# Performance work log

Measured on AMD Instinct MI355X. Metric: run time of the kernel, lower is better.

## Reference

```python
import jax, jax.numpy as jnp
import numpy as np
import math

B, T, D = 2, 4096, 2048
H, d_head, C = 16, 128, 64


def binarize(x):
    # sign to {-1,+1} with straight-through estimator (identity gradient)
    s = jnp.where(x >= 0, jnp.ones_like(x), -jnp.ones_like(x))
    return x + jax.lax.stop_gradient(s - x)


def setup_inputs() -> dict:
    key = jax.random.key(0)
    ks = jax.random.split(key, 5)
    w_std = 1.0 / math.sqrt(D)
    return {
        "x": jax.random.normal(ks[0], (B, T, D), dtype=jnp.float32),
        "Wq": jax.random.normal(ks[1], (D, D), dtype=jnp.float32) * w_std,
        "Wk": jax.random.normal(ks[2], (D, D), dtype=jnp.float32) * w_std,
        "Wv": jax.random.normal(ks[3], (D, D), dtype=jnp.float32) * w_std,
        "Wo": jax.random.normal(ks[4], (D, D), dtype=jnp.float32) * w_std,
    }


def reference(x, Wq, Wk, Wv, Wo):
    Bx, Tx, Dx = x.shape
    scale = 1.0 / math.sqrt(d_head)
    # projections (torch Linear: y = x @ W.T), split heads -> [B,H,T,d]
    q = (x @ Wq.T).reshape(Bx, Tx, H, d_head).transpose(0, 2, 1, 3) * scale
    k = binarize((x @ Wk.T).reshape(Bx, Tx, H, d_head).transpose(0, 2, 1, 3))
    v = binarize((x @ Wv.T).reshape(Bx, Tx, H, d_head).transpose(0, 2, 1, 3))
    N = Tx // C  # T chosen divisible by chunk_size
    qc = q.reshape(Bx, H, N, C, d_head)
    kc = k.reshape(Bx, H, N, C, d_head)
    vc = v.reshape(Bx, H, N, C, d_head)
    # intra-chunk causal attention
    mask = jnp.tril(jnp.ones((C, C), dtype=x.dtype))
    intra_scores = jnp.einsum('bhnid,bhnjd->bhnij', qc, kc) * mask
    intra = jnp.einsum('bhnij,bhnjd->bhnid', intra_scores, vc)
    # cross-chunk: exclusive prefix sum of per-chunk k^T v outer products
    chunk_kv = jnp.einsum('bhnci,bhncj->bhnij', kc, vc)  # [B,H,N,d,d]
    cs = jnp.cumsum(chunk_kv, axis=2)
    prefix = cs - chunk_kv  # exclusive cumsum
    cross = jnp.einsum('bhncd,bhnde->bhnce', qc, prefix)
    output = (intra + cross).reshape(Bx, H, Tx, d_head)
    out = output.transpose(0, 2, 1, 3).reshape(Bx, Tx, Dx) @ Wo.T
    final_state = cs[:, :, -1]  # [B,H,d,d]
    return out, final_state
```

## Files before the change

### kernel.cpp

```cpp
#include <hip/hip_runtime.h>
#include <stdint.h>

typedef __attribute__((ext_vector_type(8))) short short8;
typedef __attribute__((ext_vector_type(4))) float f32x4;
typedef unsigned short u16;

__device__ __forceinline__ u16 f2bf(float f) {
  uint32_t u = __builtin_bit_cast(uint32_t, f);
  u = (u + 0x7FFFu + ((u >> 16) & 1u)) >> 16;
  return (u16)u;
}
__device__ __forceinline__ float bf2f(u16 h) {
  uint32_t u = ((uint32_t)h) << 16;
  return __builtin_bit_cast(float, u);
}
__device__ __forceinline__ void lds16(const u16* g, u16* l) {
  __builtin_amdgcn_global_load_lds(
      (const __attribute__((address_space(1))) void*)g,
      (__attribute__((address_space(3))) void*)l, 16, 0, 0);
}
__device__ __forceinline__ int sw256(int i) { return i ^ (((i >> 7) & 7) << 3); }
__device__ __forceinline__ int sw128(int i) { return i ^ (((i >> 6) & 7) << 3); }
__device__ __forceinline__ int swzA64(int i) { return i ^ (((i >> 6) & 7) << 3); }
__device__ __forceinline__ int swzA32(int i) { return i ^ (((i >> 6) & 3) << 3); }

#define SB0() __builtin_amdgcn_sched_barrier(0)
#define BAR() __builtin_amdgcn_s_barrier()
#define LGKM0() do { asm volatile("s_waitcnt lgkmcnt(0)" ::: "memory"); SB0(); } while (0)
#define VM(n) asm volatile("s_waitcnt vmcnt(" #n ")" ::: "memory")
#define VMNOP do {} while (0)

__global__ __launch_bounds__(256) void split_all(
    const float* __restrict__ x,  const float* __restrict__ Wq,
    const float* __restrict__ Wk, const float* __restrict__ Wv,
    const float* __restrict__ Wo,
    u16* __restrict__ xh, u16* __restrict__ xl,
    u16* __restrict__ qh, u16* __restrict__ kh, u16* __restrict__ kl,
    u16* __restrict__ vh, u16* __restrict__ vl, u16* __restrict__ oh)
{
  const int bid = blockIdx.x, t = threadIdx.x;
  if (bid < 2048) {
    for (int i = bid * 256 + t; i < 2097152; i += 2048 * 256) {
      const float4* s = (const float4*)x + 2 * (size_t)i;
      float4 a = s[0], b = s[1];
      float v[8] = {a.x, a.y, a.z, a.w, b.x, b.y, b.z, b.w};
      short8 hi, lo;
#pragma unroll
      for (int j = 0; j < 8; j++) {
        u16 h = f2bf(v[j]);
        hi[j] = (short)h;
        lo[j] = (short)f2bf(v[j] - bf2f(h));
      }
      ((short8*)xh)[i] = hi;
      ((short8*)xl)[i] = lo;
    }
  } else {
    const int seg = (bid - 2048) >> 9;
    const int sb  = (bid - 2048) & 511;
    const float* W = seg == 0 ? Wq : seg == 1 ? Wk : seg == 2 ? Wv : Wo;
    u16* H = seg == 0 ? qh : seg == 1 ? kh : seg == 2 ? vh : oh;
    u16* L = seg == 1 ? kl : seg == 2 ? vl : nullptr;
    for (int i = sb * 256 + t; i < 524288; i += 512 * 256) {
      const float4* s = (const float4*)W + 2 * (size_t)i;
      float4 a = s[0], b = s[1];
      float v[8] = {a.x, a.y, a.z, a.w, b.x, b.y, b.z, b.w};
      short8 hi, lo;
#pragma unroll
      for (int j = 0; j < 8; j++) {
        u16 h = f2bf(v[j]);
        hi[j] = (short)h;
        lo[j] = (short)f2bf(v[j] - bf2f(h));
      }
      ((short8*)H)[i] = hi;
      if (L) ((short8*)L)[i] = lo;
    }
  }
}

template<int SPLIT, int EPI, int NTN>
__global__ __launch_bounds__(512, 2) void gemm8p(
    const u16* __restrict__ Ahi, const u16* __restrict__ Alo,
    const u16* __restrict__ Bhi, const u16* __restrict__ Blo,
    u16* __restrict__ outb, float* __restrict__ outf,
    int Mdim, int Ndim, int Kdim)
{
  constexpr int BK   = (SPLIT > 1) ? 32 : 64;
  constexpr int TILE = 256 * BK;
  constexpr int NMAT = (SPLIT > 1) ? 4 : 2;
  constexpr int AOFF_H = 0;
  constexpr int AOFF_L = (SPLIT > 1) ? TILE : 0;
  constexpr int BOFF_H = (SPLIT > 1) ? 2*TILE : TILE;
  constexpr int BOFF_L = (SPLIT > 1) ? 3*TILE : 0;
  __shared__ __align__(16) u16 smem[2 * NMAT * TILE];

  const int t = threadIdx.x, l = t & 63;
  const int w = t >> 6;
  const int wm = w >> 2, wn = w & 3;
  const int fr = l & 15, fs = l >> 4;
  const int sb = (blockIdx.x & 7) * (4 * NTN) + (blockIdx.x >> 3);
  const int m0 = (sb / NTN) * 256, n0 = (sb % NTN) * 256;
  const int NT = Kdim / BK;

  auto ST = [&](const u16* src, int g0, int moff, int kt, int r) {
    if (kt >= NT) return;
    const int bufb = (kt & 1) * NMAT * TILE;
    int d = r * 4096 + t * 8;
    int row, scol;
    if constexpr (SPLIT == 1) { row = d >> 6; scol = ((d >> 3) & 7) ^ (row & 7); }
    else                      { row = d >> 5; scol = ((d >> 3) & 3) ^ ((row >> 1) & 3); }
    lds16(src + (size_t)(g0 + row) * Kdim + kt * BK + scol * 8,
          smem + bufb + moff + d);
  };

  f32x4 acc[8][4] = {};

#define SWZ(i) ((BK == 64) ? swzA64(i) : swzA32(i))
  auto RD8 = [&](short8* dst, int bufb, int off) {
#pragma unroll
    for (int fm = 0; fm < 8; fm++) {
      int ia = (wm*128 + fm*16 + fr)*BK + fs*8;
      dst[fm] = *(const short8*)(smem + bufb + off + SWZ(ia));
    }
  };
  auto RD4 = [&](short8* dst, int bufb, int off) {
#pragma unroll
    for (int fn = 0; fn < 4; fn++) {
      int ib = (wn*64 + fn*16 + fr)*BK + fs*8;
      dst[fn] = *(const short8*)(smem + bufb + off + SWZ(ib));
    }
  };
  auto RDQ = [&](short8* dst, int bufb, int q) {
#pragma unroll
    for (int i = 0; i < 2; i++)
#pragma unroll
      for (int ks = 0; ks < 2; ks++) {
        int ia = (wm*128 + (2*q+i)*16 + fr)*64 + ks*32 + fs*8;
        dst[i*2+ks] = *(const short8*)(smem + bufb + AOFF_H + swzA64(ia));
      }
  };
  auto RDB8 = [&](short8* dst, int bufb) {
#pragma unroll
    for (int fn = 0; fn < 4; fn++)
#pragma unroll
      for (int ks = 0; ks < 2; ks++) {
        int ib = (wn*64 + fn*16 + fr)*64 + ks*32 + fs*8;
        dst[fn*2+ks] = *(const short8*)(smem + bufb + BOFF_H + swzA64(ib));
      }
  };

#define PASS32(RA, RB) do {                                                    \
  __builtin_amdgcn_s_setprio(1);                                               \
  _Pragma("unroll") for (int fm_ = 0; fm_ < 8; fm_++)                          \
    _Pragma("unroll") for (int fn_ = 0; fn_ < 4; fn_++)                        \
      acc[fm_][fn_] = __builtin_amdgcn_mfma_f32_16x16x32_bf16(                 \
          (RA)[fm_], (RB)[fn_], acc[fm_][fn_], 0, 0, 0);                       \
  __builtin_amdgcn_s_setprio(0);                                               \
  SB0();                                                                       \
} while (0)

#define PASS16(Q, AQ, BB) do {                                                 \
  __builtin_amdgcn_s_setprio(1);                                               \
  _Pragma("unroll") for (int i_ = 0; i_ < 2; i_++)                             \
    _Pragma("unroll") for (int fn_ = 0; fn_ < 4; fn_++)                        \
      _Pragma("unroll") for (int ks_ = 0; ks_ < 2; ks_++)                      \
        acc[2*(Q)+i_][fn_] = __builtin_amdgcn_mfma_f32_16x16x32_bf16(          \
            (AQ)[i_*2+ks_], (BB)[fn_*2+ks_], acc[2*(Q)+i_][fn_], 0, 0, 0);     \
  __builtin_amdgcn_s_setprio(0);                                               \
  SB0();                                                                       \
} while (0)

#define T3BODY(T, W0, W1, W2) {                                                \
  const int bufb = ((T) & 1) * NMAT * TILE;                                    \
  short8 xah[8], xbh[4], xbl[4], xal[8];                                       \
  RD8(xah, bufb, AOFF_H); RD4(xbh, bufb, BOFF_H);                              \
  ST(Ahi, m0, AOFF_H, (T)+1, 0); ST(Ahi, m0, AOFF_H, (T)+1, 1);                \
  ST(Bhi, n0, BOFF_H, (T)+1, 0); ST(Bhi, n0, BOFF_H, (T)+1, 1);                \
  W0; BAR(); LGKM0(); PASS32(xah, xbh); BAR();                                 \
  RD4(xbl, bufb, BOFF_L);                                                      \
  ST(Blo, n0, BOFF_L, (T)+1, 0); ST(Blo, n0, BOFF_L, (T)+1, 1);                \
  W1; BAR(); LGKM0(); PASS32(xah, xbl); BAR();                                 \
  RD8(xal, bufb, AOFF_L);                                                      \
  ST(Alo, m0, AOFF_L, (T)+1, 0); ST(Alo, m0, AOFF_L, (T)+1, 1);                \
  W2; BAR(); LGKM0(); PASS32(xal, xbh); BAR();                                 \
}

#define T1BODY(T, W1, W3) {                                                    \
  const int bufb = ((T) & 1) * NMAT * TILE;                                    \
  short8 bb[8], aq[4];                                                         \
  RDB8(bb, bufb); RDQ(aq, bufb, 0);                                            \
  ST(Bhi, n0, BOFF_H, (T)+1, 0); ST(Bhi, n0, BOFF_H, (T)+1, 1);                \
  BAR(); LGKM0(); PASS16(0, aq, bb); BAR();                                    \
  RDQ(aq, bufb, 1);                                                            \
  ST(Bhi, n0, BOFF_H, (T)+1, 2); ST(Bhi, n0, BOFF_H, (T)+1, 3);                \
  W1; BAR(); LGKM0(); PASS16(1, aq, bb); BAR();                                \
  RDQ(aq, bufb, 2);                                                            \
  ST(Ahi, m0, AOFF_H, (T)+1, 0); ST(Ahi, m0, AOFF_H, (T)+1, 2);                \
  BAR(); LGKM0(); PASS16(2, aq, bb); BAR();                                    \
  RDQ(aq, bufb, 3);                                                            \
  ST(Ahi, m0, AOFF_H, (T)+1, 1); ST(Ahi, m0, AOFF_H, (T)+1, 3);                \
  W3; BAR(); LGKM0(); PASS16(3, aq, bb); BAR();                                \
}

  if constexpr (SPLIT > 1) {
    ST(Ahi, m0, AOFF_H, 0, 0); ST(Ahi, m0, AOFF_H, 0, 1);
    ST(Bhi, n0, BOFF_H, 0, 0); ST(Bhi, n0, BOFF_H, 0, 1);
    ST(Blo, n0, BOFF_L, 0, 0); ST(Blo, n0, BOFF_L, 0, 1);
    ST(Alo, m0, AOFF_L, 0, 0); ST(Alo, m0, AOFF_L, 0, 1);
    VM(4); BAR();
    for (int T = 0; T < NT - 1; T++) T3BODY(T, VM(6), VM(6), VM(4))
    T3BODY(NT - 1, VM(2), VM(0), VMNOP)
  } else {
    ST(Bhi, n0, BOFF_H, 0, 0); ST(Bhi, n0, BOFF_H, 0, 1);
    ST(Bhi, n0, BOFF_H, 0, 2); ST(Bhi, n0, BOFF_H, 0, 3);
    ST(Ahi, m0, AOFF_H, 0, 0); ST(Ahi, m0, AOFF_H, 0, 2);
    ST(Ahi, m0, AOFF_H, 0, 1); ST(Ahi, m0, AOFF_H, 0, 3);
    VM(2); BAR();
    for (int T = 0; T < NT - 1; T++) T1BODY(T, VM(4), VM(2))
    T1BODY(NT - 1, VM(0), VMNOP)
  }
#undef SWZ
#undef T3BODY
#undef T1BODY
#undef PASS32
#undef PASS16

  const float qscale = 0.08838834764831843f;
#pragma unroll
  for (int fm = 0; fm < 8; fm++)
#pragma unroll
    for (int fn = 0; fn < 4; fn++)
#pragma unroll
      for (int r = 0; r < 4; r++) {
        int gm = m0 + wm*128 + fm*16 + fs*4 + r;
        int gn = n0 + wn*64 + fn*16 + fr;
        float val = acc[fm][fn][r];
        if constexpr (EPI == 2) {
          outf[(size_t)gm * Ndim + gn] = val;
        } else if constexpr (EPI == 0) {
          int b = gm >> 12, tt = gm & 4095, h = gn >> 7, dd = gn & 127;
          size_t idx = (((size_t)(b*16 + h))*4096 + tt)*128 + dd;
          outb[idx] = f2bf(val * qscale);
        } else {
          int b = gm >> 12, tt = gm & 4095;
          int kv = gn >> 11, h = (gn >> 7) & 15, dd = gn & 127;
          size_t idx = (size_t)kv * 16777216 +
                       (((size_t)(b*16 + h))*4096 + tt)*128 + dd;
          outb[idx] = (val >= 0.f) ? (u16)0x3F80 : (u16)0xBF80;
        }
      }
}

__global__ void pack_signs(const u16* __restrict__ k, const u16* __restrict__ v,
                           unsigned long long* __restrict__ kp, unsigned long long* __restrict__ vp) {
  const int blk = blockIdx.x;
  const int d = threadIdx.x;
  const int bh = blk >> 6, n = blk & 63;
  size_t base = (((size_t)bh * 4096) + n * 64) * 128 + d;
  unsigned long long kw = 0, vw = 0;
  for (int c = 0; c < 64; c++) {
    kw |= (unsigned long long)(k[base + (size_t)c*128] >> 15) << c;
    vw |= (unsigned long long)(v[base + (size_t)c*128] >> 15) << c;
  }
  kp[(size_t)blk * 128 + d] = kw;
  vp[(size_t)blk * 128 + d] = vw;
}

__global__ __launch_bounds__(256) void scan_kernel(
    const unsigned long long* __restrict__ kp, const unsigned long long* __restrict__ vp,
    short* __restrict__ pfx8, float* __restrict__ fsT)
{
  const int t = threadIdx.x;
  const int bh = blockIdx.x >> 6, ep = blockIdx.x & 63;
  const int e = ep * 2 + (t >> 7), d = t & 127;
  const size_t base = (size_t)bh * 64 * 128;
  int s = 0;
  for (int n = 0; n < 64; n++) {
    if ((n & 7) == 0)
      pfx8[((size_t)(bh*8 + (n>>3))*128 + e)*128 + d] = (short)s;
    unsigned long long kw = kp[base + (size_t)n*128 + d];
    unsigned long long vw = vp[base + (size_t)n*128 + e];
    s += 64 - 2*__popcll(kw ^ vw);
  }
  fsT[((size_t)bh*128 + e)*128 + d] = (float)s;
}

__global__ __launch_bounds__(256) void transpose_fs(const float* __restrict__ fsT,
                                                    float* __restrict__ fstate) {
  __shared__ float tile[32*130];
  const int t = threadIdx.x;
  const int bh = blockIdx.x >> 2, es = (blockIdx.x & 3) * 32;
#pragma unroll
  for (int i = 0; i < 16; i++) {
    int idx = t + i*256;
    int e2 = idx >> 7, d = idx & 127;
    tile[e2*130 + d] = fsT[((size_t)bh*128 + es + e2)*128 + d];
  }
  __syncthreads();
#pragma unroll
  for (int i = 0; i < 16; i++) {
    int idx = t + i*256;
    int d = idx >> 5, e2 = idx & 31;
    fstate[((size_t)bh*128 + d)*128 + es + e2] = tile[e2*130 + d];
  }
}

__global__ __launch_bounds__(256) void fused_attn(
    const u16* __restrict__ q, const u16* __restrict__ k,
    const unsigned long long* __restrict__ kp, const unsigned long long* __restrict__ vp,
    const short* __restrict__ pfx8, u16* __restrict__ att)
{
  __shared__ __align__(16) u16 smem[28672];
  u16* sQ  = smem;
  u16* sP1 = smem + 8192;
  u16* sP2 = smem + 16384;
  u16* sS  = smem + 24576;

  const int t = threadIdx.x, l = t & 63, w = t >> 6;
  const int blk = blockIdx.x, bh = blk >> 6, n = blk & 63;
  const int b = bh >> 4, hh = bh & 15;
  const int fr = l & 15, fs = l >> 4;
  const size_t qbase = (((size_t)bh * 4096) + n * 64) * 128;
  const size_t pbase = (size_t)bh * 64 * 128;

#pragma unroll
  for (int i = 0; i < 4; i++) {
    int arow = i*16 + (t>>4);
    int aslot = (t & 15) ^ (arow & 7);
    size_t g = qbase + (size_t)arow*128 + aslot*8;
    lds16(q + g, sQ + i*2048 + t*8);
    lds16(k + g, sP1 + i*2048 + t*8);
  }
  {
    int d = t >> 1, ch = (t & 1) * 32;
    unsigned long long wv = vp[pbase + (size_t)n*128 + d];
#pragma unroll
    for (int c = 0; c < 32; c += 2) {
      uint32_t b0 = ((wv >> (ch + c)) & 1ull)     ? 0xBF80u : 0x3F80u;
      uint32_t b1 = ((wv >> (ch + c + 1)) & 1ull) ? 0xBF80u : 0x3F80u;
      int li = d*64 + ch + c;
      *(uint32_t*)(sP2 + sw128(li)) = b0 | (b1 << 16);
    }
  }
  __syncthreads();

  f32x4 accS[4] = {};
#pragma unroll
  for (int kk = 0; kk < 4; kk++) {
    int la = (w*16 + fr)*128 + kk*32 + fs*8;
    short8 a = *(const short8*)(sQ + sw256(la));
#pragma unroll
    for (int fn = 0; fn < 4; fn++) {
      int lb = (fn*16 + fr)*128 + kk*32 + fs*8;
      short8 bb = *(const short8*)(sP1 + sw256(lb));
      accS[fn] = __builtin_amdgcn_mfma_f32_16x16x32_bf16(a, bb, accS[fn], 0, 0, 0);
    }
  }
#pragma unroll
  for (int fn = 0; fn < 4; fn++)
#pragma unroll
    for (int r = 0; r < 4; r++) {
      int i = w*16 + fs*4 + r, j = fn*16 + fr;
      float v = (j <= i) ? accS[fn][r] : 0.f;
      sS[sw128(i*64 + j)] = f2bf(v);
    }
  __syncthreads();

  f32x4 accI[8] = {};
#pragma unroll
  for (int kk = 0; kk < 2; kk++) {
    int la = (w*16 + fr)*64 + kk*32 + fs*8;
    short8 a = *(const short8*)(sS + sw128(la));
#pragma unroll
    for (int fn = 0; fn < 8; fn++) {
      int lb = (fn*16 + fr)*64 + kk*32 + fs*8;
      short8 bb = *(const short8*)(sP2 + sw128(lb));
      accI[fn] = __builtin_amdgcn_mfma_f32_16x16x32_bf16(a, bb, accI[fn], 0, 0, 0);
    }
  }
  __syncthreads();

  const int m0 = n & ~7, cnt = n & 7;
  for (int hf = 0; hf < 2; hf++) {
#pragma unroll
    for (int p = 0; p < 4; p++) {
      int erow = p*16 + (t>>4);
      int e = hf*64 + erow;
      const short* ps = pfx8 + ((size_t)(bh*8 + (n>>3))*128 + e)*128 + (t&15)*8;
      short8 pv = *(const short8*)ps;
      int accj[8];
#pragma unroll
      for (int j = 0; j < 8; j++) accj[j] = pv[j];
      for (int m = 0; m < cnt; m++) {
        unsigned long long vw = vp[pbase + (size_t)(m0+m)*128 + e];
#pragma unroll
        for (int j = 0; j < 8; j++) {
          unsigned long long kw = kp[pbase + (size_t)(m0+m)*128 + (t&15)*8 + j];
          accj[j] += 64 - 2*__popcll(kw ^ vw);
        }
      }
      short8 hi, lo;
#pragma unroll
      for (int j = 0; j < 8; j++) {
        hi[j] = (short)f2bf((float)(accj[j] >> 5));
        lo[j] = (short)f2bf((float)(accj[j] & 31));
      }
      int pi = sw256(erow*128 + (t&15)*8);
      *(short8*)(sP1 + pi) = hi;
      *(short8*)(sP2 + pi) = lo;
    }
    __syncthreads();

    f32x4 acch[4] = {}, accl[4] = {};
#pragma unroll
    for (int kk = 0; kk < 4; kk++) {
      int la = (w*16 + fr)*128 + kk*32 + fs*8;
      short8 a = *(const short8*)(sQ + sw256(la));
#pragma unroll
      for (int fn = 0; fn < 4; fn++) {
        int pb = sw256((fn*16 + fr)*128 + kk*32 + fs*8);
        acch[fn] = __builtin_amdgcn_mfma_f32_16x16x32_bf16(a, *(const short8*)(sP1 + pb), acch[fn], 0, 0, 0);
        accl[fn] = __builtin_amdgcn_mfma_f32_16x16x32_bf16(a, *(const short8*)(sP2 + pb), accl[fn], 0, 0, 0);
      }
    }
#pragma unroll
    for (int fn = 0; fn < 4; fn++)
#pragma unroll
      for (int r = 0; r < 4; r++) {
        int c = w*16 + fs*4 + r;
        int dcol = hf*64 + fn*16 + fr;
        float val = accI[hf*4+fn][r] + 32.f*acch[fn][r] + accl[fn][r];
        size_t idx = ((size_t)(b*4096 + n*64 + c))*2048 + hh*128 + dcol;
        att[idx] = f2bf(val);
      }
    __syncthreads();
  }
}

extern "C" void kernel_launch(void* const* d_in, const int* in_sizes, int n_in,
                              void* d_out, int out_size, void* d_ws, size_t ws_size,
                              hipStream_t stream) {
  (void)in_sizes; (void)n_in; (void)out_size; (void)ws_size;
  const float* x  = (const float*)d_in[0];
  const float* Wq = (const float*)d_in[1];
  const float* Wk = (const float*)d_in[2];
  const float* Wv = (const float*)d_in[3];
  const float* Wo = (const float*)d_in[4];
  float* out = (float*)d_out;
  float* fstate = out + (size_t)16777216;

  char* ws = (char*)d_ws;
  u16* x_hi = (u16*)(ws + 0);
  u16* x_lo = (u16*)(ws + 33554432);
  u16* qb   = (u16*)(ws + 67108864);
  u16* kb   = (u16*)(ws + 100663296);
  u16* vb   = (u16*)(ws + 134217728);
  u16* wq_h  = (u16*)(ws + 167772160);
  u16* wkv_h = (u16*)(ws + 176160768);
  u16* wkv_l = (u16*)(ws + 192937984);
  u16* wo_h  = (u16*)(ws + 209715200);
  unsigned long long* kpk = (unsigned long long*)(ws + 218103808);
  unsigned long long* vpk = (unsigned long long*)(ws + 220200960);
  u16* att    = x_hi;
  float* fsT  = (float*)(ws + 33554432);
  short* pfx8 = (short*)(ws + 134217728);

  split_all<<<4096, 256, 0, stream>>>(x, Wq, Wk, Wv, Wo,
                                      x_hi, x_lo, wq_h,
                                      wkv_h, wkv_l,
                                      wkv_h + 4194304, wkv_l + 4194304,
                                      wo_h);

  gemm8p<1,0,8><<<256, 512, 0, stream>>>(x_hi, nullptr, wq_h, nullptr, qb, nullptr, 8192, 2048, 2048);
  gemm8p<3,1,16><<<512, 512, 0, stream>>>(x_hi, x_lo, wkv_h, wkv_l, kb, nullptr, 8192, 4096, 2048);

  pack_signs<<<2048, 128, 0, stream>>>(kb, vb, kpk, vpk);
  scan_kernel<<<2048, 256, 0, stream>>>(kpk, vpk, pfx8, fsT);
  transpose_fs<<<128, 256, 0, stream>>>(fsT, fstate);
  fused_attn<<<2048, 256, 0, stream>>>(qb, kb, kpk, vpk, pfx8, att);

  gemm8p<1,2,8><<<256, 512, 0, stream>>>(att, nullptr, wo_h, nullptr, nullptr, out, 8192, 2048, 2048);
}
```

Before: 667.2 us.

## Fuse sign-bit packing into K/V projection GEMM epilogue via wave ballots

```diff
diff --git a/kernel.cpp b/kernel.cpp
--- a/kernel.cpp
+++ b/kernel.cpp
@@ -4,6 +4,7 @@
 typedef __attribute__((ext_vector_type(8))) short short8;
 typedef __attribute__((ext_vector_type(4))) float f32x4;
 typedef unsigned short u16;
+typedef unsigned long long u64;
 
 __device__ __forceinline__ u16 f2bf(float f) {
   uint32_t u = __builtin_bit_cast(uint32_t, f);
@@ -82,6 +83,7 @@
     const u16* __restrict__ Ahi, const u16* __restrict__ Alo,
     const u16* __restrict__ Bhi, const u16* __restrict__ Blo,
     u16* __restrict__ outb, float* __restrict__ outf,
+    u64* __restrict__ kpk_p, u64* __restrict__ vpk_p,
     int Mdim, int Ndim, int Kdim)
 {
   constexpr int BK   = (SPLIT > 1) ? 32 : 64;
@@ -224,49 +226,61 @@
 #undef PASS32
 #undef PASS16
 
-  const float qscale = 0.08838834764831843f;
-#pragma unroll
-  for (int fm = 0; fm < 8; fm++)
-#pragma unroll
-    for (int fn = 0; fn < 4; fn++)
-#pragma unroll
-      for (int r = 0; r < 4; r++) {
-        int gm = m0 + wm*128 + fm*16 + fs*4 + r;
-        int gn = n0 + wn*64 + fn*16 + fr;
-        float val = acc[fm][fn][r];
-        if constexpr (EPI == 2) {
-          outf[(size_t)gm * Ndim + gn] = val;
-        } else if constexpr (EPI == 0) {
-          int b = gm >> 12, tt = gm & 4095, h = gn >> 7, dd = gn & 127;
-          size_t idx = (((size_t)(b*16 + h))*4096 + tt)*128 + dd;
-          outb[idx] = f2bf(val * qscale);
-        } else {
-          int b = gm >> 12, tt = gm & 4095;
+  if constexpr (EPI == 1) {
+#pragma unroll
+    for (int q = 0; q < 2; q++) {
+#pragma unroll
+      for (int fn = 0; fn < 4; fn++) {
+        u64 bal[4][4];
+#pragma unroll
+        for (int j = 0; j < 4; j++)
+#pragma unroll
+          for (int r = 0; r < 4; r++)
+            bal[j][r] = __ballot(acc[4*q + j][fn][r] < 0.f);
+        if (l < 16) {
+          u64 wq = 0;
+#pragma unroll
+          for (int j = 0; j < 4; j++)
+#pragma unroll
+            for (int r = 0; r < 4; r++) {
+              u64 x = (bal[j][r] >> l) & 0x0001000100010001ULL;
+              u64 y = (x & 1) | ((x >> 12) & 0x10) |
+                      ((x >> 24) & 0x100) | ((x >> 36) & 0x1000);
+              wq |= y << (j*16 + r);
+            }
+          int gmc = m0 + wm*128 + q*64;
+          int gn  = n0 + wn*64 + fn*16 + l;
+          int b = gmc >> 12, n = (gmc & 4095) >> 6;
           int kv = gn >> 11, h = (gn >> 7) & 15, dd = gn & 127;
-          size_t idx = (size_t)kv * 16777216 +
-                       (((size_t)(b*16 + h))*4096 + tt)*128 + dd;
-          outb[idx] = (val >= 0.f) ? (u16)0x3F80 : (u16)0xBF80;
+          u64* dst = kv ? vpk_p : kpk_p;
+          dst[((size_t)((b*16 + h)*64 + n))*128 + dd] = wq;
         }
       }
-}
-
-__global__ void pack_signs(const u16* __restrict__ k, const u16* __restrict__ v,
-                           unsigned long long* __restrict__ kp, unsigned long long* __restrict__ vp) {
-  const int blk = blockIdx.x;
-  const int d = threadIdx.x;
-  const int bh = blk >> 6, n = blk & 63;
-  size_t base = (((size_t)bh * 4096) + n * 64) * 128 + d;
-  unsigned long long kw = 0, vw = 0;
-  for (int c = 0; c < 64; c++) {
-    kw |= (unsigned long long)(k[base + (size_t)c*128] >> 15) << c;
-    vw |= (unsigned long long)(v[base + (size_t)c*128] >> 15) << c;
-  }
-  kp[(size_t)blk * 128 + d] = kw;
-  vp[(size_t)blk * 128 + d] = vw;
+    }
+  } else {
+    const float qscale = 0.08838834764831843f;
+#pragma unroll
+    for (int fm = 0; fm < 8; fm++)
+#pragma unroll
+      for (int fn = 0; fn < 4; fn++)
+#pragma unroll
+        for (int r = 0; r < 4; r++) {
+          int gm = m0 + wm*128 + fm*16 + fs*4 + r;
+          int gn = n0 + wn*64 + fn*16 + fr;
+          float val = acc[fm][fn][r];
+          if constexpr (EPI == 2) {
+            outf[(size_t)gm * Ndim + gn] = val;
+          } else {
+            int b = gm >> 12, tt = gm & 4095, h = gn >> 7, dd = gn & 127;
+            size_t idx = (((size_t)(b*16 + h))*4096 + tt)*128 + dd;
+            outb[idx] = f2bf(val * qscale);
+          }
+        }
+  }
 }
 
 __global__ __launch_bounds__(256) void scan_kernel(
-    const unsigned long long* __restrict__ kp, const unsigned long long* __restrict__ vp,
+    const u64* __restrict__ kp, const u64* __restrict__ vp,
     short* __restrict__ pfx8, float* __restrict__ fsT)
 {
   const int t = threadIdx.x;
@@ -277,8 +291,8 @@
   for (int n = 0; n < 64; n++) {
     if ((n & 7) == 0)
       pfx8[((size_t)(bh*8 + (n>>3))*128 + e)*128 + d] = (short)s;
-    unsigned long long kw = kp[base + (size_t)n*128 + d];
-    unsigned long long vw = vp[base + (size_t)n*128 + e];
+    u64 kw = kp[base + (size_t)n*128 + d];
+    u64 vw = vp[base + (size_t)n*128 + e];
     s += 64 - 2*__popcll(kw ^ vw);
   }
   fsT[((size_t)bh*128 + e)*128 + d] = (float)s;
@@ -305,8 +319,8 @@
 }
 
 __global__ __launch_bounds__(256) void fused_attn(
-    const u16* __restrict__ q, const u16* __restrict__ k,
-    const unsigned long long* __restrict__ kp, const unsigned long long* __restrict__ vp,
+    const u16* __restrict__ q,
+    const u64* __restrict__ kp, const u64* __restrict__ vp,
     const short* __restrict__ pfx8, u16* __restrict__ att)
 {
   __shared__ __align__(16) u16 smem[28672];
@@ -328,11 +342,22 @@
     int aslot = (t & 15) ^ (arow & 7);
     size_t g = qbase + (size_t)arow*128 + aslot*8;
     lds16(q + g, sQ + i*2048 + t*8);
-    lds16(k + g, sP1 + i*2048 + t*8);
+  }
+  {
+    const u64* krow = kp + pbase + (size_t)n*128;
+    int d = (t & 63) * 2, c0 = (t >> 6) * 16;
+    u64 w0 = krow[d], w1 = krow[d+1];
+#pragma unroll
+    for (int i = 0; i < 16; i++) {
+      int c = c0 + i;
+      uint32_t b0 = ((w0 >> c) & 1ull) ? 0xBF80u : 0x3F80u;
+      uint32_t b1 = ((w1 >> c) & 1ull) ? 0xBF80u : 0x3F80u;
+      *(uint32_t*)(sP1 + sw256(c*128 + d)) = b0 | (b1 << 16);
+    }
   }
   {
     int d = t >> 1, ch = (t & 1) * 32;
-    unsigned long long wv = vp[pbase + (size_t)n*128 + d];
+    u64 wv = vp[pbase + (size_t)n*128 + d];
 #pragma unroll
     for (int c = 0; c < 32; c += 2) {
       uint32_t b0 = ((wv >> (ch + c)) & 1ull)     ? 0xBF80u : 0x3F80u;
@@ -391,10 +416,10 @@
 #pragma unroll
       for (int j = 0; j < 8; j++) accj[j] = pv[j];
       for (int m = 0; m < cnt; m++) {
-        unsigned long long vw = vp[pbase + (size_t)(m0+m)*128 + e];
+        u64 vw = vp[pbase + (size_t)(m0+m)*128 + e];
 #pragma unroll
         for (int j = 0; j < 8; j++) {
-          unsigned long long kw = kp[pbase + (size_t)(m0+m)*128 + (t&15)*8 + j];
+          u64 kw = kp[pbase + (size_t)(m0+m)*128 + (t&15)*8 + j];
           accj[j] += 64 - 2*__popcll(kw ^ vw);
         }
       }
@@ -452,14 +477,12 @@
   u16* x_hi = (u16*)(ws + 0);
   u16* x_lo = (u16*)(ws + 33554432);
   u16* qb   = (u16*)(ws + 67108864);
-  u16* kb   = (u16*)(ws + 100663296);
-  u16* vb   = (u16*)(ws + 134217728);
   u16* wq_h  = (u16*)(ws + 167772160);
   u16* wkv_h = (u16*)(ws + 176160768);
   u16* wkv_l = (u16*)(ws + 192937984);
   u16* wo_h  = (u16*)(ws + 209715200);
-  unsigned long long* kpk = (unsigned long long*)(ws + 218103808);
-  unsigned long long* vpk = (unsigned long long*)(ws + 220200960);
+  u64* kpk = (u64*)(ws + 218103808);
+  u64* vpk = (u64*)(ws + 220200960);
   u16* att    = x_hi;
   float* fsT  = (float*)(ws + 33554432);
   short* pfx8 = (short*)(ws + 134217728);
@@ -470,13 +493,15 @@
                                       wkv_h + 4194304, wkv_l + 4194304,
                                       wo_h);
 
-  gemm8p<1,0,8><<<256, 512, 0, stream>>>(x_hi, nullptr, wq_h, nullptr, qb, nullptr, 8192, 2048, 2048);
-  gemm8p<3,1,16><<<512, 512, 0, stream>>>(x_hi, x_lo, wkv_h, wkv_l, kb, nullptr, 8192, 4096, 2048);
-
-  pack_signs<<<2048, 128, 0, stream>>>(kb, vb, kpk, vpk);
+  gemm8p<1,0,8><<<256, 512, 0, stream>>>(x_hi, nullptr, wq_h, nullptr, qb, nullptr,
+                                         nullptr, nullptr, 8192, 2048, 2048);
+  gemm8p<3,1,16><<<512, 512, 0, stream>>>(x_hi, x_lo, wkv_h, wkv_l, nullptr, nullptr,
+                                          kpk, vpk, 8192, 4096, 2048);
+
   scan_kernel<<<2048, 256, 0, stream>>>(kpk, vpk, pfx8, fsT);
   transpose_fs<<<128, 256, 0, stream>>>(fsT, fstate);
-  fused_attn<<<2048, 256, 0, stream>>>(qb, kb, kpk, vpk, pfx8, att);
-
-  gemm8p<1,2,8><<<256, 512, 0, stream>>>(att, nullptr, wo_h, nullptr, nullptr, out, 8192, 2048, 2048);
-}
+  fused_attn<<<2048, 256, 0, stream>>>(qb, kpk, vpk, pfx8, att);
+
+  gemm8p<1,2,8><<<256, 512, 0, stream>>>(att, nullptr, wo_h, nullptr, nullptr, out,
+                                         nullptr, nullptr, 8192, 2048, 2048);
+}
```

New measurement: 653.2 us. 2.1% less time.
